# Performance work log

Hardware: AMD Instinct MI355X
Metric: run time of the kernel (lower is better)

Reference implementation:

```python
import jax, jax.numpy as jnp
import numpy as np

N, E, G = 50000, 1600000, 64          # nodes, edges, graphs
NODE_IN, EDGE_IN, HID, L, H = 32, 16, 64, 3, 4
C = HID // H                           # per-head channels (PyG out_channels)


def setup_inputs() -> dict:
    key = jax.random.key(0)
    ks = jax.random.split(key, 12)
    x = jax.random.normal(ks[0], (N, NODE_IN), jnp.float32)
    edge_index = jax.random.randint(ks[1], (2, E), 0, N, jnp.int32)
    edge_attr = jax.random.normal(ks[2], (E, EDGE_IN), jnp.float32)
    batch = jnp.sort(jax.random.randint(ks[3], (N,), 0, G, jnp.int32))
    s = lambda k, shape, fan: jax.random.normal(k, shape, jnp.float32) / np.sqrt(fan)
    Wn = s(ks[4], (NODE_IN, HID), NODE_IN); bn = jnp.zeros((HID,), jnp.float32)
    Wq = s(ks[5], (L, HID, HID), HID);      bq = jnp.zeros((L, HID), jnp.float32)
    Wk = s(ks[6], (L, HID, HID), HID);      bk = jnp.zeros((L, HID), jnp.float32)
    Wv = s(ks[7], (L, HID, HID), HID);      bv = jnp.zeros((L, HID), jnp.float32)
    We = s(ks[8], (L, EDGE_IN, HID), EDGE_IN)          # lin_edge, bias=False in PyG
    Ws = s(ks[9], (L, HID, HID), HID);      bs = jnp.zeros((L, HID), jnp.float32)  # lin_skip
    W1 = s(ks[10], (HID, HID // 2), HID);   b1 = jnp.zeros((HID // 2,), jnp.float32)
    W2 = s(ks[11], (HID // 2, 1), HID // 2); b2 = jnp.zeros((1,), jnp.float32)
    return dict(x=x, edge_index=edge_index, edge_attr=edge_attr, batch=batch,
                Wn=Wn, bn=bn, Wq=Wq, bq=bq, Wk=Wk, bk=bk, Wv=Wv, bv=bv,
                We=We, Ws=Ws, bs=bs, W1=W1, b1=b1, W2=W2, b2=b2)


def _transformer_conv(x, src, dst, edge_attr, Wq, bq, Wk, bk, Wv, bv, We, Ws, bs):
    # PyG TransformerConv (concat=True, beta=False, root_weight=True), eval mode.
    q = (x @ Wq + bq)[dst].reshape(E, H, C)              # query at target nodes
    e = (edge_attr @ We).reshape(E, H, C)                # edge embedding
    k = (x @ Wk + bk)[src].reshape(E, H, C) + e          # key at source + edge
    alpha = (q * k).sum(-1) / jnp.sqrt(jnp.float32(C))   # [E, H]
    amax = jax.ops.segment_max(alpha, dst, num_segments=N)
    ex = jnp.exp(alpha - amax[dst])
    denom = jax.ops.segment_sum(ex, dst, num_segments=N)
    attn = ex / (denom[dst] + 1e-16)                     # segment softmax over in-edges
    v = (x @ Wv + bv)[src].reshape(E, H, C) + e
    agg = jax.ops.segment_sum((v * attn[..., None]).reshape(E, HID), dst, num_segments=N)
    return agg + x @ Ws + bs                             # skip connection (lin_skip)


def reference(x, edge_index, edge_attr, batch, Wn, bn, Wq, bq, Wk, bk, Wv, bv,
              We, Ws, bs, W1, b1, W2, b2):
    src, dst = edge_index[0], edge_index[1]
    h = jax.nn.relu(x @ Wn + bn)
    for l in range(L):  # dropout is identity in eval mode
        h_new = jax.nn.relu(_transformer_conv(h, src, dst, edge_attr,
                                              Wq[l], bq[l], Wk[l], bk[l],
                                              Wv[l], bv[l], We[l], Ws[l], bs[l]))
        h = h + h_new
    # global_mean_pool
    cnt = jax.ops.segment_sum(jnp.ones((N,), h.dtype), batch, num_segments=G)
    pooled = jax.ops.segment_sum(h, batch, num_segments=G) / jnp.maximum(cnt, 1.0)[:, None]
    out = jax.nn.relu(pooled @ W1 + b1) @ W2 + b2
    return out.squeeze(-1)
```

## Files before the change

kernel.cpp:

```cpp
#include <hip/hip_runtime.h>
#include <hip/hip_fp16.h>
#include <stdint.h>

#define Nn 50000
#define Ee 1600000
#define Gg 64
#define TB 2048
#define NTB ((Ee + TB - 1) / TB)
#define NBK ((Nn + 255) / 256)

typedef _Float16 f16x2 __attribute__((ext_vector_type(2)));
typedef _Float16 f16x4 __attribute__((ext_vector_type(4)));
typedef _Float16 f16x8 __attribute__((ext_vector_type(8)));
typedef float    f32x4v __attribute__((ext_vector_type(4)));

__device__ __forceinline__ float fdot2f(f16x2 a, f16x2 b, float c) {
#if __has_builtin(__builtin_amdgcn_fdot2)
    return __builtin_amdgcn_fdot2(a, b, c, false);
#else
    return fmaf((float)a[0], (float)b[0], fmaf((float)a[1], (float)b[1], c));
#endif
}

__global__ void k_hist(const int* __restrict__ ei, int* __restrict__ deg) {
    int e = blockIdx.x * blockDim.x + threadIdx.x;
    if (e < Ee) atomicAdd(&deg[ei[Ee + e]], 1);
}

__global__ void k_scan1(const int* __restrict__ deg, int* __restrict__ row_ptr,
                        int* __restrict__ bsum) {
    __shared__ int buf[256];
    int i = blockIdx.x * 256 + threadIdx.x;
    int v = (i < Nn) ? deg[i] : 0;
    buf[threadIdx.x] = v;
    __syncthreads();
    for (int off = 1; off < 256; off <<= 1) {
        int t = (threadIdx.x >= off) ? buf[threadIdx.x - off] : 0;
        __syncthreads();
        buf[threadIdx.x] += t;
        __syncthreads();
    }
    if (i < Nn) row_ptr[i + 1] = buf[threadIdx.x];
    if (threadIdx.x == 255) bsum[blockIdx.x] = buf[255];
}

__global__ void k_scan2(int* __restrict__ bsum, int nb) {
    __shared__ int buf[256];
    int v = (threadIdx.x < nb) ? bsum[threadIdx.x] : 0;
    buf[threadIdx.x] = v;
    __syncthreads();
    for (int off = 1; off < 256; off <<= 1) {
        int t = (threadIdx.x >= off) ? buf[threadIdx.x - off] : 0;
        __syncthreads();
        buf[threadIdx.x] += t;
        __syncthreads();
    }
    if (threadIdx.x < nb) bsum[threadIdx.x] = buf[threadIdx.x];
}

__global__ void k_scan3(int* __restrict__ row_ptr, const int* __restrict__ bsum) {
    int i = blockIdx.x * 256 + threadIdx.x;
    if (i > Nn) return;
    if (i == 0) { row_ptr[0] = 0; return; }
    int b = (i - 1) >> 8;
    if (b > 0) row_ptr[i] += bsum[b - 1];
}

__global__ void k_scatter(const int* __restrict__ ei, int* __restrict__ cursor,
                          int* __restrict__ src_perm, int* __restrict__ eperm) {
    int e = blockIdx.x * blockDim.x + threadIdx.x;
    if (e >= Ee) return;
    int dst = ei[Ee + e];
    int pos = atomicAdd(&cursor[dst], 1);
    src_perm[pos] = ei[e];
    eperm[pos] = e;
}

__global__ void k_easort(const float* __restrict__ ea, const int* __restrict__ eperm,
                         __half* __restrict__ ea_h) {
    long t = (long)blockIdx.x * blockDim.x + threadIdx.x;
    if (t >= (long)Ee * 4) return;
    long idx = t >> 2;
    int e = eperm[idx];
    float4 v = ((const float4*)ea)[(long)e * 4 + (t & 3)];
    __half2 lo = __floats2half2_rn(v.x, v.y);
    __half2 hi = __floats2half2_rn(v.z, v.w);
    ((__half2*)ea_h)[t * 2]     = lo;
    ((__half2*)ea_h)[t * 2 + 1] = hi;
}


__global__ __launch_bounds__(256) void k_cnt(const int* __restrict__ ei,
                                             int* __restrict__ table) {
    __shared__ int hist[NBK];
    for (int i = threadIdx.x; i < NBK; i += 256) hist[i] = 0;
    __syncthreads();
    int e0 = blockIdx.x * TB;
    for (int i = threadIdx.x; i < TB; i += 256) {
        int e = e0 + i;
        if (e >= Ee) break;
        atomicAdd(&hist[ei[Ee + e] >> 8], 1);
    }
    __syncthreads();
    for (int i = threadIdx.x; i < NBK; i += 256)
        table[i * NTB + blockIdx.x] = hist[i];
}

__global__ __launch_bounds__(256) void k_colscan(int* __restrict__ table,
                                                 int* __restrict__ bktsz) {
    __shared__ int buf[1024];
    int c = blockIdx.x;
    for (int k = 0; k < 4; ++k) {
        int i = threadIdx.x + k * 256;
        buf[i] = (i < NTB) ? table[c * NTB + i] : 0;
    }
    __syncthreads();
    for (int off = 1; off < 1024; off <<= 1) {
        int v[4];
        for (int k = 0; k < 4; ++k) {
            int i = threadIdx.x + k * 256;
            v[k] = (i >= off) ? buf[i - off] : 0;
        }
        __syncthreads();
        for (int k = 0; k < 4; ++k) buf[threadIdx.x + k * 256] += v[k];
        __syncthreads();
    }
    for (int k = 0; k < 4; ++k) {
        int i = threadIdx.x + k * 256;
        if (i < NTB) table[c * NTB + i] = i ? buf[i - 1] : 0;
    }
    if (threadIdx.x == 0) bktsz[c] = buf[1023];
}

__global__ __launch_bounds__(256) void k_bktscan(const int* __restrict__ bktsz,
                                                 int* __restrict__ bktbase) {
    __shared__ int buf[256];
    int i = threadIdx.x;
    buf[i] = (i < NBK) ? bktsz[i] : 0;
    __syncthreads();
    for (int off = 1; off < 256; off <<= 1) {
        int v = (i >= off) ? buf[i - off] : 0;
        __syncthreads();
        buf[i] += v;
        __syncthreads();
    }
    if (i == 0) bktbase[0] = 0;
    if (i < NBK) bktbase[i + 1] = buf[i];
}

__global__ __launch_bounds__(256) void k_binfill(const int* __restrict__ ei,
                        const int* __restrict__ table, const int* __restrict__ bktbase,
                        unsigned long long* __restrict__ tmp) {
    __shared__ int off_s[NBK];
    __shared__ int cnt_s[NBK];
    for (int i = threadIdx.x; i < NBK; i += 256) {
        off_s[i] = table[i * NTB + blockIdx.x];
        cnt_s[i] = 0;
    }
    __syncthreads();
    int e0 = blockIdx.x * TB;
    for (int i = threadIdx.x; i < TB; i += 256) {
        int e = e0 + i;
        if (e >= Ee) break;
        int src = ei[e];
        int dst = ei[Ee + e];
        int b = dst >> 8;
        int r = atomicAdd(&cnt_s[b], 1);
        long pos = (long)bktbase[b] + off_s[b] + r;
        tmp[pos] = ((unsigned long long)(unsigned)dst << 37)
                 | ((unsigned long long)(unsigned)src << 21)
                 | (unsigned long long)(unsigned)e;
    }
}

__global__ __launch_bounds__(256) void k_bktB(const unsigned long long* __restrict__ tmp,
                        const int* __restrict__ bktbase, int* __restrict__ row_ptr,
                        int* __restrict__ src_perm, int* __restrict__ eord) {
    __shared__ int cnt[256];
    __shared__ int sc[256];
    __shared__ int lro[256];
    int b = blockIdx.x, tid = threadIdx.x;
    cnt[tid] = 0;
    __syncthreads();
    int s = bktbase[b], t_end = bktbase[b + 1];
    for (int i = s + tid; i < t_end; i += 256)
        atomicAdd(&cnt[(int)(tmp[i] >> 37) & 255], 1);
    __syncthreads();
    sc[tid] = cnt[tid];
    __syncthreads();
    for (int off = 1; off < 256; off <<= 1) {
        int v = (tid >= off) ? sc[tid - off] : 0;
        __syncthreads();
        sc[tid] += v;
        __syncthreads();
    }
    lro[tid] = tid ? sc[tid - 1] : 0;
    cnt[tid] = 0;
    int n = b * 256 + tid;
    if (n < Nn) row_ptr[n] = s + lro[tid];
    if (b == NBK - 1 && tid == 0) row_ptr[Nn] = Ee;
    __syncthreads();
    for (int i = s + tid; i < t_end; i += 256) {
        unsigned long long p = tmp[i];
        int dn = (int)(p >> 37) & 255;
        int r = atomicAdd(&cnt[dn], 1);
        int pos = s + lro[dn] + r;
        src_perm[pos] = (int)((p >> 21) & 0xFFFFull);
        eord[pos] = (int)(p & 0x1FFFFFull);
    }
}

__global__ void k_scatB2(const int* __restrict__ eord,
                         const float* __restrict__ ea, __half* __restrict__ ea_h) {
    int t = blockIdx.x * blockDim.x + threadIdx.x;
    if (t >= Ee) return;
    int e = eord[t];
    const f32x4v* er = (const f32x4v*)(ea + (size_t)e * 16);
    f32x4v v0 = __builtin_nontemporal_load(er);
    f32x4v v1 = __builtin_nontemporal_load(er + 1);
    f32x4v v2 = __builtin_nontemporal_load(er + 2);
    f32x4v v3 = __builtin_nontemporal_load(er + 3);
    __half2 h0 = __floats2half2_rn(v0[0], v0[1]), h1 = __floats2half2_rn(v0[2], v0[3]);
    __half2 h2 = __floats2half2_rn(v1[0], v1[1]), h3 = __floats2half2_rn(v1[2], v1[3]);
    __half2 h4 = __floats2half2_rn(v2[0], v2[1]), h5 = __floats2half2_rn(v2[2], v2[3]);
    __half2 h6 = __floats2half2_rn(v3[0], v3[1]), h7 = __floats2half2_rn(v3[2], v3[3]);
    uint4 a = make_uint4(*(unsigned*)&h0, *(unsigned*)&h1,
                         *(unsigned*)&h2, *(unsigned*)&h3);
    uint4 bb = make_uint4(*(unsigned*)&h4, *(unsigned*)&h5,
                          *(unsigned*)&h6, *(unsigned*)&h7);
    uint4* o = (uint4*)(ea_h + (size_t)t * 16);
    o[0] = a;
    o[1] = bb;
}

__global__ void k_gbound(const int* __restrict__ batch, int* __restrict__ gstart) {
    int n = blockIdx.x * blockDim.x + threadIdx.x;
    if (n >= Nn) return;
    int b = batch[n];
    if (n == 0) { for (int g = 0; g <= b; ++g) gstart[g] = 0; }
    else { int bp = batch[n - 1]; for (int g = bp + 1; g <= b; ++g) gstart[g] = n; }
    if (n == Nn - 1) { for (int g = b + 1; g <= Gg; ++g) gstart[g] = Nn; }
}

__global__ __launch_bounds__(256) void k_encode(const float* __restrict__ x,
                         const float* __restrict__ Wn,
                         const float* __restrict__ bn, float* __restrict__ h) {
    __shared__ float sx[64 * 32];
    int base = blockIdx.x * 64;
    for (int i = threadIdx.x; i < 512; i += 256) {
        int off = i * 4, row = off >> 5;
        float4 v = (base + row < Nn) ? ((const float4*)(x))[(base * 32 + off) >> 2]
                                     : make_float4(0.f, 0.f, 0.f, 0.f);
        ((float4*)sx)[i] = v;
    }
    __syncthreads();
    int lane = threadIdx.x & 63, wv = threadIdx.x >> 6;
    float acc[16];
    float b = bn[lane];
#pragma unroll
    for (int nn = 0; nn < 16; ++nn) acc[nn] = b;
#pragma unroll 1
    for (int k0 = 0; k0 < 32; k0 += 4) {
        float w0 = Wn[(k0 + 0) * 64 + lane];
        float w1 = Wn[(k0 + 1) * 64 + lane];
        float w2 = Wn[(k0 + 2) * 64 + lane];
        float w3 = Wn[(k0 + 3) * 64 + lane];
#pragma unroll
        for (int nn = 0; nn < 16; ++nn) {
            int row = wv * 16 + nn;
            float4 hv = *(const float4*)&sx[row * 32 + k0];
            acc[nn] = fmaf(hv.x, w0, fmaf(hv.y, w1, fmaf(hv.z, w2, fmaf(hv.w, w3, acc[nn]))));
        }
    }
#pragma unroll
    for (int nn = 0; nn < 16; ++nn) {
        int n = base + wv * 16 + nn;
        if (n < Nn) h[(size_t)n * 64 + lane] = fmaxf(acc[nn], 0.f);
    }
}

__global__ void k_wqm3(const float* __restrict__ Wq_all, const float* __restrict__ bq_all,
                       const float* __restrict__ We_all, float* __restrict__ Wqm3,
                       float* __restrict__ bqm3) {
    int l = blockIdx.x;
    const float* Wq = Wq_all + l * 4096;
    const float* bq = bq_all + l * 64;
    const float* We = We_all + l * 1024;
    float* Wqm = Wqm3 + l * 4096;
    float* bqm = bqm3 + l * 64;
    for (int o = threadIdx.x; o < 64 * 64; o += 256) {
        int j = o >> 6, lp = o & 63, hh = lp >> 4, ii = lp & 15;
        float acc = 0.f;
#pragma unroll
        for (int c = 0; c < 16; ++c)
            acc += Wq[j * 64 + hh * 16 + c] * We[ii * 64 + hh * 16 + c];
        Wqm[o] = acc;
    }
    if (threadIdx.x < 64) {
        int hh = threadIdx.x >> 4, ii = threadIdx.x & 15;
        float acc = 0.f;
#pragma unroll
        for (int c = 0; c < 16; ++c)
            acc += bq[hh * 16 + c] * We[ii * 64 + hh * 16 + c];
        bqm[threadIdx.x] = acc;
    }
}

__global__ void k_pack(const float* __restrict__ Wq, const float* __restrict__ Wk,
                       const float* __restrict__ Wv, const float* __restrict__ Wqm3,
                       const float* __restrict__ Ws, __half* __restrict__ pw) {
    int l = blockIdx.x / 5, m = blockIdx.x % 5;
    const float SC = 0.25f * 1.4426950408889634f;
    const float* src;
    float sc = 1.f;
    if (m == 0)      { src = Wq + l * 4096;   sc = SC; }
    else if (m == 1) { src = Wk + l * 4096; }
    else if (m == 2) { src = Wv + l * 4096; }
    else if (m == 3) { src = Wqm3 + l * 4096; sc = SC; }
    else             { src = Ws + l * 4096; }
    __half* dst = pw + ((size_t)l * 5 + m) * 4096;
    for (int i = threadIdx.x; i < 4096; i += 256) {
        int k = i >> 6, c = i & 63;
        dst[(k >> 1) * 128 + 2 * c + (k & 1)] = __float2half_rn(src[i] * sc);
    }
}

__global__ __launch_bounds__(256) void k_qkvt2(const float* __restrict__ h,
                       const __half* __restrict__ pw,
                       const float* __restrict__ bq, const float* __restrict__ bk,
                       const float* __restrict__ bv, const float* __restrict__ bqm,
                       const float* __restrict__ bs,
                       __half* __restrict__ qn16, __half* __restrict__ kvi,
                       __half* __restrict__ tq16, float* __restrict__ sn) {
    __shared__ __half sh[64 * 64];
    int base = blockIdx.x * 64;
    for (int i = threadIdx.x; i < 1024; i += 256) {
        int off = i * 4, row = off >> 6;
        float4 v = (base + row < Nn) ? ((const float4*)(h))[((size_t)base * 64 + off) >> 2]
                                     : make_float4(0.f, 0.f, 0.f, 0.f);
        ((__half2*)sh)[i * 2]     = __floats2half2_rn(v.x, v.y);
        ((__half2*)sh)[i * 2 + 1] = __floats2half2_rn(v.z, v.w);
    }
    __syncthreads();
    int lane = threadIdx.x & 63, wv = threadIdx.x >> 6;
    const float SC = 0.25f * 1.4426950408889634f;
    const __half* Pq = pw;
    const __half* Pk = pw + 4096;
    const __half* Pv = pw + 8192;
    const __half* Pt = pw + 12288;
    const __half* Ps = pw + 16384;
    float aq[16], ak[16], av[16], at[16], as_[16];
    float _bq = bq[lane] * SC, _bk = bk[lane], _bv = bv[lane],
          _bt = bqm[lane] * SC, _bs = bs[lane];
#pragma unroll
    for (int nn = 0; nn < 16; ++nn) {
        aq[nn] = _bq; ak[nn] = _bk; av[nn] = _bv; at[nn] = _bt; as_[nn] = _bs;
    }
#pragma unroll 1
    for (int k0 = 0; k0 < 64; k0 += 4) {
        int pi = (k0 >> 1) * 128 + 2 * lane;
        f16x2 wq0 = *(const f16x2*)(Pq + pi), wq1 = *(const f16x2*)(Pq + pi + 128);
        f16x2 wk0 = *(const f16x2*)(Pk + pi), wk1 = *(const f16x2*)(Pk + pi + 128);
        f16x2 wv0 = *(const f16x2*)(Pv + pi), wv1 = *(const f16x2*)(Pv + pi + 128);
        f16x2 wt0 = *(const f16x2*)(Pt + pi), wt1 = *(const f16x2*)(Pt + pi + 128);
        f16x2 ws0 = *(const f16x2*)(Ps + pi), ws1 = *(const f16x2*)(Ps + pi + 128);
#pragma unroll
        for (int nn = 0; nn < 16; ++nn) {
            int row = wv * 16 + nn;
            f16x4 hv = *(const f16x4*)&sh[row * 64 + k0];
            f16x2 h01 = __builtin_shufflevector(hv, hv, 0, 1);
            f16x2 h23 = __builtin_shufflevector(hv, hv, 2, 3);
            aq[nn]  = fdot2f(h01, wq0, fdot2f(h23, wq1, aq[nn]));
            ak[nn]  = fdot2f(h01, wk0, fdot2f(h23, wk1, ak[nn]));
            av[nn]  = fdot2f(h01, wv0, fdot2f(h23, wv1, av[nn]));
            at[nn]  = fdot2f(h01, wt0, fdot2f(h23, wt1, at[nn]));
            as_[nn] = fdot2f(h01, ws0, fdot2f(h23, ws1, as_[nn]));
        }
    }
    int ko = 8 * (lane >> 2) + (lane & 3);
#pragma unroll
    for (int nn = 0; nn < 16; ++nn) {
        int n = base + wv * 16 + nn;
        if (n < Nn) {
            size_t o = (size_t)n * 64 + lane;
            qn16[o] = __float2half_rn(aq[nn]);
            tq16[o] = __float2half_rn(at[nn]);
            sn[o] = as_[nn];
            kvi[(size_t)n * 128 + ko]     = __float2half_rn(ak[nn]);
            kvi[(size_t)n * 128 + ko + 4] = __float2half_rn(av[nn]);
        }
    }
}

__global__ __launch_bounds__(256) void k_layer8(float* __restrict__ h,
                      const __half* __restrict__ qn16, const __half* __restrict__ kvi,
                      const __half* __restrict__ tq16, const float* __restrict__ sn,
                      const int* __restrict__ row_ptr, const int* __restrict__ src_perm,
                      const __half* __restrict__ eah, const float* __restrict__ We) {
    __shared__ float sWe[1024];
    __shared__ float tE[4][64];
    __shared__ float tV[4][64];
    for (int t = threadIdx.x; t < 1024; t += 256) sWe[t] = We[t];
    __syncthreads();
    int lane = threadIdx.x & 63, wv = threadIdx.x >> 6;
    int slot = lane >> 4, sl = lane & 15;
    int hh = lane >> 4;
    const int xoff = 4 * (sl & 3);
#pragma unroll 1
    for (int j = 0; j < 4; ++j) {
        int n = blockIdx.x * 16 + wv * 4 + j;
        if (n >= Nn) break;
        int beg = row_ptr[n], end = row_ptr[n + 1];
        f16x4 qv = *(const f16x4*)(qn16 + (size_t)n * 64 + 4 * sl);
        f16x4 tv = *(const f16x4*)(tq16 + (size_t)n * 64 + 4 * sl);
        f16x2 qa = __builtin_shufflevector(qv, qv, 0, 1);
        f16x2 qb = __builtin_shufflevector(qv, qv, 2, 3);
        f16x2 ta = __builtin_shufflevector(tv, tv, 0, 1);
        f16x2 tb = __builtin_shufflevector(tv, tv, 2, 3);
        float accd = 0.f;
        float4 accv = make_float4(0.f, 0.f, 0.f, 0.f);
        float4 acce = make_float4(0.f, 0.f, 0.f, 0.f);
        for (int idx = beg; idx < end; idx += 8) {
            int e0 = idx + slot, e1 = idx + 4 + slot;
            bool ok0 = e0 < end, ok1 = e1 < end;
            int i0 = ok0 ? e0 : beg, i1 = ok1 ? e1 : beg;
            int s0 = src_perm[i0], s1 = src_perm[i1];
            f16x8 kv0 = *(const f16x8*)(kvi + (size_t)s0 * 128 + 8 * sl);
            f16x8 kv1 = *(const f16x8*)(kvi + (size_t)s1 * 128 + 8 * sl);
            f16x4 x0 = *(const f16x4*)(eah + (size_t)i0 * 16 + xoff);
            f16x4 x1 = *(const f16x4*)(eah + (size_t)i1 * 16 + xoff);
            float a0 = fdot2f(qa, __builtin_shufflevector(kv0, kv0, 0, 1),
                       fdot2f(qb, __builtin_shufflevector(kv0, kv0, 2, 3),
                       fdot2f(ta, __builtin_shufflevector(x0, x0, 0, 1),
                       fdot2f(tb, __builtin_shufflevector(x0, x0, 2, 3), -6.0f))));
            float a1 = fdot2f(qa, __builtin_shufflevector(kv1, kv1, 0, 1),
                       fdot2f(qb, __builtin_shufflevector(kv1, kv1, 2, 3),
                       fdot2f(ta, __builtin_shufflevector(x1, x1, 0, 1),
                       fdot2f(tb, __builtin_shufflevector(x1, x1, 2, 3), -6.0f))));
            a0 += __shfl_xor(a0, 1, 4); a1 += __shfl_xor(a1, 1, 4);
            a0 += __shfl_xor(a0, 2, 4); a1 += __shfl_xor(a1, 2, 4);
            float p0 = ok0 ? __builtin_exp2f(a0) : 0.f;
            float p1 = ok1 ? __builtin_exp2f(a1) : 0.f;
            accd += p0 + p1;
            accv.x = fmaf(p0, (float)kv0[4], fmaf(p1, (float)kv1[4], accv.x));
            accv.y = fmaf(p0, (float)kv0[5], fmaf(p1, (float)kv1[5], accv.y));
            accv.z = fmaf(p0, (float)kv0[6], fmaf(p1, (float)kv1[6], accv.z));
            accv.w = fmaf(p0, (float)kv0[7], fmaf(p1, (float)kv1[7], accv.w));
            acce.x = fmaf(p0, (float)x0[0], fmaf(p1, (float)x1[0], acce.x));
            acce.y = fmaf(p0, (float)x0[1], fmaf(p1, (float)x1[1], acce.y));
            acce.z = fmaf(p0, (float)x0[2], fmaf(p1, (float)x1[2], acce.z));
            acce.w = fmaf(p0, (float)x0[3], fmaf(p1, (float)x1[3], acce.w));
        }
        accd   += __shfl_xor(accd, 16);   accd   += __shfl_xor(accd, 32);
        accv.x += __shfl_xor(accv.x, 16); accv.x += __shfl_xor(accv.x, 32);
        accv.y += __shfl_xor(accv.y, 16); accv.y += __shfl_xor(accv.y, 32);
        accv.z += __shfl_xor(accv.z, 16); accv.z += __shfl_xor(accv.z, 32);
        accv.w += __shfl_xor(accv.w, 16); accv.w += __shfl_xor(accv.w, 32);
        acce.x += __shfl_xor(acce.x, 16); acce.x += __shfl_xor(acce.x, 32);
        acce.y += __shfl_xor(acce.y, 16); acce.y += __shfl_xor(acce.y, 32);
        acce.z += __shfl_xor(acce.z, 16); acce.z += __shfl_xor(acce.z, 32);
        acce.w += __shfl_xor(acce.w, 16); acce.w += __shfl_xor(acce.w, 32);
        float inv = 1.f / (accd + 1e-16f);
        if (slot == 0) {
            ((float4*)tE[wv])[sl] = make_float4(acce.x * inv, acce.y * inv,
                                                acce.z * inv, acce.w * inv);
            ((float4*)tV[wv])[sl] = make_float4(accv.x * inv, accv.y * inv,
                                                accv.z * inv, accv.w * inv);
        }
        float re = 0.f;
#pragma unroll
        for (int i = 0; i < 16; ++i)
            re = fmaf(tE[wv][hh * 16 + i], sWe[i * 64 + lane], re);
        size_t o = (size_t)n * 64 + lane;
        float hv = h[o];
        h[o] = hv + fmaxf(tV[wv][lane] + re + sn[o], 0.f);
    }
}

__global__ __launch_bounds__(256) void k_layer(float* __restrict__ h,
                      const __half* __restrict__ qn16, const __half* __restrict__ kvi,
                      const __half* __restrict__ tq16, const float* __restrict__ sn,
                      const int* __restrict__ row_ptr, const int* __restrict__ src_perm,
                      const int* __restrict__ eperm, const float* __restrict__ eaf,
                      const float* __restrict__ We) {
    __shared__ float sWe[1024];
    __shared__ float tile[4][64];
    for (int t = threadIdx.x; t < 1024; t += 256) sWe[t] = We[t];
    __syncthreads();
    int lane = threadIdx.x & 63, wv = threadIdx.x >> 6;
    int hh = lane >> 4, cc = lane & 15;
    int ko = 8 * (lane >> 2) + (lane & 3);
    int n = blockIdx.x * 4 + wv;
    if (n >= Nn) return;
    int beg = row_ptr[n], end = row_ptr[n + 1];
    float q = __half2float(qn16[(size_t)n * 64 + lane]);
    float t = __half2float(tq16[(size_t)n * 64 + lane]);
    float m = -INFINITY, accd = 0.f, accv = 0.f, acce = 0.f;
    int idx = beg;
    for (; idx < end; ++idx) {
        long b0 = (long)src_perm[idx] * 128;
        float k0 = __half2float(kvi[b0 + ko]);
        float v0 = __half2float(kvi[b0 + ko + 4]);
        float x0 = eaf[(long)eperm[idx] * 16 + cc];
        float a0 = fmaf(q, k0, x0 * t);
        a0 += __shfl_xor(a0, 1, 16);
        a0 += __shfl_xor(a0, 2, 16);
        a0 += __shfl_xor(a0, 4, 16);
        a0 += __shfl_xor(a0, 8, 16);
        float nm = fmaxf(m, a0);
        float w = __builtin_exp2f(m - nm);
        float p0 = __builtin_exp2f(a0 - nm);
        accd = fmaf(accd, w, p0);
        accv = fmaf(accv, w, p0 * v0);
        acce = fmaf(acce, w, p0 * x0);
        m = nm;
    }
    float inv = 1.f / (accd + 1e-16f);
    tile[wv][lane] = acce * inv;
    float re = 0.f;
#pragma unroll
    for (int i = 0; i < 16; ++i)
        re = fmaf(tile[wv][hh * 16 + i], sWe[i * 64 + lane], re);
    size_t o = (size_t)n * 64 + lane;
    float hv = h[o];
    h[o] = hv + fmaxf(fmaf(accv, inv, re + sn[o]), 0.f);
}

__global__ void k_pool(const float* __restrict__ h, const int* __restrict__ gstart,
                       const float* __restrict__ W1, const float* __restrict__ b1,
                       const float* __restrict__ W2, const float* __restrict__ b2,
                       float* __restrict__ out) {
    int g = blockIdx.x;
    int lane = threadIdx.x & 63, wv = threadIdx.x >> 6;
    int beg = gstart[g], end = gstart[g + 1];
    __shared__ float red[4][64];
    __shared__ float sp[64];
    __shared__ float sh[32];
    float acc = 0.f;
    for (int n = beg + wv; n < end; n += 4) acc += h[(size_t)n * 64 + lane];
    red[wv][lane] = acc;
    __syncthreads();
    if (threadIdx.x < 64) {
        float c = fmaxf((float)(end - beg), 1.f);
        sp[lane] = (red[0][lane] + red[1][lane] + red[2][lane] + red[3][lane]) / c;
    }
    __syncthreads();
    if (threadIdx.x < 32) {
        int t = threadIdx.x;
        float a = b1[t];
#pragma unroll
        for (int i = 0; i < 64; ++i) a = fmaf(sp[i], W1[i * 32 + t], a);
        sh[t] = fmaxf(a, 0.f) * W2[t];
    }
    __syncthreads();
    if (threadIdx.x == 0) {
        float s = b2[0];
#pragma unroll
        for (int i = 0; i < 32; ++i) s += sh[i];
        out[g] = s;
    }
}

extern "C" void kernel_launch(void* const* d_in, const int* in_sizes, int n_in,
                              void* d_out, int out_size, void* d_ws, size_t ws_size,
                              hipStream_t stream) {
    const float* x   = (const float*)d_in[0];
    const int*   ei  = (const int*)d_in[1];
    const float* ea  = (const float*)d_in[2];
    const int*   bat = (const int*)d_in[3];
    const float* Wn  = (const float*)d_in[4];
    const float* bn  = (const float*)d_in[5];
    const float* Wq  = (const float*)d_in[6];
    const float* bq  = (const float*)d_in[7];
    const float* Wk  = (const float*)d_in[8];
    const float* bk  = (const float*)d_in[9];
    const float* Wv  = (const float*)d_in[10];
    const float* bv  = (const float*)d_in[11];
    const float* We  = (const float*)d_in[12];
    const float* Wsk = (const float*)d_in[13];
    const float* bs  = (const float*)d_in[14];
    const float* W1  = (const float*)d_in[15];
    const float* b1  = (const float*)d_in[16];
    const float* W2  = (const float*)d_in[17];
    const float* b2  = (const float*)d_in[18];
    float* out = (float*)d_out;

    const size_t NH = (size_t)Nn * 64;
    float* h    = (float*)d_ws;
    float* qn   = h + NH;
    float* tq   = h + 2 * NH;
    float* sn   = h + 3 * NH;
    __half* kv  = (__half*)(h + 4 * NH);
    float* Wqm3 = h + 5 * NH;
    float* bqm3 = Wqm3 + 3 * 4096;
    __half* pw  = (__half*)(bqm3 + 3 * 64);
    int* deg       = (int*)(pw + 3 * 5 * 4096);
    int* row_ptr   = deg + Nn;
    int* cursor    = row_ptr + Nn + 1;
    int* src_perm  = cursor + Nn;
    int* eperm     = src_perm + Ee;
    int* bsum      = eperm + Ee;
    int* gstart    = bsum + 256;
    char* pe = (char*)(gstart + Gg + 1);
    __half* ea_h = (__half*)(((uintptr_t)pe + 63) & ~(uintptr_t)63);
    char* pt = (char*)(ea_h + (size_t)Ee * 16);
    unsigned long long* tmp =
        (unsigned long long*)(((uintptr_t)pt + 15) & ~(uintptr_t)15);
    size_t need_eah = ((char*)(ea_h + (size_t)Ee * 16)) - (char*)d_ws;
    size_t need_tmp = ((char*)(tmp + Ee)) - (char*)d_ws;
    int* eord    = (int*)qn;
    int* table   = (int*)tq;
    int* bktsz   = (int*)sn;
    int* bktbase = bktsz + 256;
    __half* qn16 = (__half*)qn;
    __half* tq16 = (__half*)tq;
    int mode = (ws_size >= need_tmp) ? 2 : (ws_size >= need_eah) ? 1 : 0;

    if (mode == 2) {
        k_cnt<<<NTB, 256, 0, stream>>>(ei, table);
        k_colscan<<<NBK, 256, 0, stream>>>(table, bktsz);
        k_bktscan<<<1, 256, 0, stream>>>(bktsz, bktbase);
        k_binfill<<<NTB, 256, 0, stream>>>(ei, table, bktbase, tmp);
        k_bktB<<<NBK, 256, 0, stream>>>(tmp, bktbase, row_ptr, src_perm, eord);
        k_scatB2<<<(Ee + 255) / 256, 256, 0, stream>>>(eord, ea, ea_h);
    } else {
        const int NB = 196;
        hipMemsetAsync(deg, 0, Nn * sizeof(int), stream);
        k_hist<<<(Ee + 255) / 256, 256, 0, stream>>>(ei, deg);
        k_scan1<<<NB, 256, 0, stream>>>(deg, row_ptr, bsum);
        k_scan2<<<1, 256, 0, stream>>>(bsum, NB);
        k_scan3<<<(Nn + 256) / 256, 256, 0, stream>>>(row_ptr, bsum);
        hipMemcpyAsync(cursor, row_ptr, Nn * sizeof(int), hipMemcpyDeviceToDevice, stream);
        k_scatter<<<(Ee + 255) / 256, 256, 0, stream>>>(ei, cursor, src_perm, eperm);
        if (mode == 1)
            k_easort<<<((long)Ee * 4 + 255) / 256, 256, 0, stream>>>(ea, eperm, ea_h);
    }
    k_gbound<<<(Nn + 255) / 256, 256, 0, stream>>>(bat, gstart);
    k_wqm3<<<3, 256, 0, stream>>>(Wq, bq, We, Wqm3, bqm3);
    k_pack<<<15, 256, 0, stream>>>(Wq, Wk, Wv, Wqm3, Wsk, pw);

    int nodeBlocks = (Nn + 63) / 64;
    k_encode<<<nodeBlocks, 256, 0, stream>>>(x, Wn, bn, h);
    for (int l = 0; l < 3; ++l) {
        k_qkvt2<<<nodeBlocks, 256, 0, stream>>>(h, pw + (size_t)l * 5 * 4096,
                                                bq + l * 64, bk + l * 64, bv + l * 64,
                                                bqm3 + l * 64, bs + l * 64,
                                                qn16, kv, tq16, sn);
        if (mode >= 1)
            k_layer8<<<(Nn + 15) / 16, 256, 0, stream>>>(h, qn16, kv, tq16, sn,
                    row_ptr, src_perm, ea_h, We + l * 1024);
        else
            k_layer<<<(Nn + 3) / 4, 256, 0, stream>>>(h, qn16, kv, tq16, sn,
                    row_ptr, src_perm, eperm, ea, We + l * 1024);
    }
    k_pool<<<Gg, 256, 0, stream>>>(h, gstart, W1, b1, W2, b2, out);
}
```

Baseline: 683.5 us.

## Use 64-node buckets and fuse edge-attr scatter with layer-0 QKV kernel

Shrinks the CSR bucket granularity from 256 to 64 destination nodes, so there are four times as many buckets and the bucket-scan grows to 1024 entries. k_bktB now runs with only 64 active counters per block. The edge-attribute scatter/fp16 conversion now handles two edges per thread with plain loads instead of nontemporal ones. It is merged with the first layer's QKV projection into a single launch that runs both concurrently via a block-index split, with eord moved to eperm so it no longer aliases qn. Fewer bins and more blocks improve parallelism in the bucket phase, but three quarters of the threads in k_bktB sit idle during the scan.

```diff
diff --git a/kernel.cpp b/kernel.cpp
--- a/kernel.cpp
+++ b/kernel.cpp
@@ -7,12 +7,12 @@
 #define Gg 64
 #define TB 2048
 #define NTB ((Ee + TB - 1) / TB)
-#define NBK ((Nn + 255) / 256)
+#define NBK ((Nn + 63) / 64)
+#define SB2B 3125
 
 typedef _Float16 f16x2 __attribute__((ext_vector_type(2)));
 typedef _Float16 f16x4 __attribute__((ext_vector_type(4)));
 typedef _Float16 f16x8 __attribute__((ext_vector_type(8)));
-typedef float    f32x4v __attribute__((ext_vector_type(4)));
 
 __device__ __forceinline__ float fdot2f(f16x2 a, f16x2 b, float c) {
 #if __has_builtin(__builtin_amdgcn_fdot2)
@@ -99,7 +99,7 @@
     for (int i = threadIdx.x; i < TB; i += 256) {
         int e = e0 + i;
         if (e >= Ee) break;
-        atomicAdd(&hist[ei[Ee + e] >> 8], 1);
+        atomicAdd(&hist[ei[Ee + e] >> 6], 1);
     }
     __syncthreads();
     for (int i = threadIdx.x; i < NBK; i += 256)
@@ -134,18 +134,27 @@
 
 __global__ __launch_bounds__(256) void k_bktscan(const int* __restrict__ bktsz,
                                                  int* __restrict__ bktbase) {
-    __shared__ int buf[256];
-    int i = threadIdx.x;
-    buf[i] = (i < NBK) ? bktsz[i] : 0;
-    __syncthreads();
-    for (int off = 1; off < 256; off <<= 1) {
-        int v = (i >= off) ? buf[i - off] : 0;
-        __syncthreads();
-        buf[i] += v;
-        __syncthreads();
-    }
-    if (i == 0) bktbase[0] = 0;
-    if (i < NBK) bktbase[i + 1] = buf[i];
+    __shared__ int buf[1024];
+    for (int k = 0; k < 4; ++k) {
+        int i = threadIdx.x + k * 256;
+        buf[i] = (i < NBK) ? bktsz[i] : 0;
+    }
+    __syncthreads();
+    for (int off = 1; off < 1024; off <<= 1) {
+        int v[4];
+        for (int k = 0; k < 4; ++k) {
+            int i = threadIdx.x + k * 256;
+            v[k] = (i >= off) ? buf[i - off] : 0;
+        }
+        __syncthreads();
+        for (int k = 0; k < 4; ++k) buf[threadIdx.x + k * 256] += v[k];
+        __syncthreads();
+    }
+    for (int k = 0; k < 4; ++k) {
+        int i = threadIdx.x + k * 256;
+        if (i < NBK) bktbase[i + 1] = buf[i];
+    }
+    if (threadIdx.x == 0) bktbase[0] = 0;
 }
 
 __global__ __launch_bounds__(256) void k_binfill(const int* __restrict__ ei,
@@ -164,7 +173,7 @@
         if (e >= Ee) break;
         int src = ei[e];
         int dst = ei[Ee + e];
-        int b = dst >> 8;
+        int b = dst >> 6;
         int r = atomicAdd(&cnt_s[b], 1);
         long pos = (long)bktbase[b] + off_s[b] + r;
         tmp[pos] = ((unsigned long long)(unsigned)dst << 37)
@@ -176,33 +185,35 @@
 __global__ __launch_bounds__(256) void k_bktB(const unsigned long long* __restrict__ tmp,
                         const int* __restrict__ bktbase, int* __restrict__ row_ptr,
                         int* __restrict__ src_perm, int* __restrict__ eord) {
-    __shared__ int cnt[256];
-    __shared__ int sc[256];
-    __shared__ int lro[256];
+    __shared__ int cnt[64];
+    __shared__ int sc[64];
+    __shared__ int lro[64];
     int b = blockIdx.x, tid = threadIdx.x;
-    cnt[tid] = 0;
+    if (tid < 64) cnt[tid] = 0;
     __syncthreads();
     int s = bktbase[b], t_end = bktbase[b + 1];
     for (int i = s + tid; i < t_end; i += 256)
-        atomicAdd(&cnt[(int)(tmp[i] >> 37) & 255], 1);
-    __syncthreads();
-    sc[tid] = cnt[tid];
-    __syncthreads();
-    for (int off = 1; off < 256; off <<= 1) {
-        int v = (tid >= off) ? sc[tid - off] : 0;
-        __syncthreads();
-        sc[tid] += v;
-        __syncthreads();
-    }
-    lro[tid] = tid ? sc[tid - 1] : 0;
-    cnt[tid] = 0;
-    int n = b * 256 + tid;
-    if (n < Nn) row_ptr[n] = s + lro[tid];
+        atomicAdd(&cnt[(int)(tmp[i] >> 37) & 63], 1);
+    __syncthreads();
+    if (tid < 64) sc[tid] = cnt[tid];
+    __syncthreads();
+    for (int off = 1; off < 64; off <<= 1) {
+        int v = (tid < 64 && tid >= off) ? sc[tid - off] : 0;
+        __syncthreads();
+        if (tid < 64) sc[tid] += v;
+        __syncthreads();
+    }
+    if (tid < 64) {
+        lro[tid] = tid ? sc[tid - 1] : 0;
+        cnt[tid] = 0;
+        int n = b * 64 + tid;
+        if (n < Nn) row_ptr[n] = s + lro[tid];
+    }
     if (b == NBK - 1 && tid == 0) row_ptr[Nn] = Ee;
     __syncthreads();
     for (int i = s + tid; i < t_end; i += 256) {
         unsigned long long p = tmp[i];
-        int dn = (int)(p >> 37) & 255;
+        int dn = (int)(p >> 37) & 63;
         int r = atomicAdd(&cnt[dn], 1);
         int pos = s + lro[dn] + r;
         src_perm[pos] = (int)((p >> 21) & 0xFFFFull);
@@ -210,27 +221,33 @@
     }
 }
 
+__device__ __forceinline__ void scatB2_body(int bid, const int* __restrict__ eord,
+                        const float* __restrict__ ea, __half* __restrict__ ea_h) {
+    int t0 = (bid * 256 + threadIdx.x) * 2;
+    if (t0 >= Ee) return;
+    int e0 = eord[t0], e1 = eord[t0 + 1];
+    const float4* r0 = (const float4*)(ea + (size_t)e0 * 16);
+    const float4* r1 = (const float4*)(ea + (size_t)e1 * 16);
+    float4 a0 = r0[0], a1 = r0[1], a2 = r0[2], a3 = r0[3];
+    float4 c0 = r1[0], c1 = r1[1], c2 = r1[2], c3 = r1[3];
+    __half2 h0 = __floats2half2_rn(a0.x, a0.y), h1 = __floats2half2_rn(a0.z, a0.w);
+    __half2 h2 = __floats2half2_rn(a1.x, a1.y), h3 = __floats2half2_rn(a1.z, a1.w);
+    __half2 h4 = __floats2half2_rn(a2.x, a2.y), h5 = __floats2half2_rn(a2.z, a2.w);
+    __half2 h6 = __floats2half2_rn(a3.x, a3.y), h7 = __floats2half2_rn(a3.z, a3.w);
+    __half2 g0 = __floats2half2_rn(c0.x, c0.y), g1 = __floats2half2_rn(c0.z, c0.w);
+    __half2 g2 = __floats2half2_rn(c1.x, c1.y), g3 = __floats2half2_rn(c1.z, c1.w);
+    __half2 g4 = __floats2half2_rn(c2.x, c2.y), g5 = __floats2half2_rn(c2.z, c2.w);
+    __half2 g6 = __floats2half2_rn(c3.x, c3.y), g7 = __floats2half2_rn(c3.z, c3.w);
+    uint4* o = (uint4*)(ea_h + (size_t)t0 * 16);
+    o[0] = make_uint4(*(unsigned*)&h0, *(unsigned*)&h1, *(unsigned*)&h2, *(unsigned*)&h3);
+    o[1] = make_uint4(*(unsigned*)&h4, *(unsigned*)&h5, *(unsigned*)&h6, *(unsigned*)&h7);
+    o[2] = make_uint4(*(unsigned*)&g0, *(unsigned*)&g1, *(unsigned*)&g2, *(unsigned*)&g3);
+    o[3] = make_uint4(*(unsigned*)&g4, *(unsigned*)&g5, *(unsigned*)&g6, *(unsigned*)&g7);
+}
+
 __global__ void k_scatB2(const int* __restrict__ eord,
                          const float* __restrict__ ea, __half* __restrict__ ea_h) {
-    int t = blockIdx.x * blockDim.x + threadIdx.x;
-    if (t >= Ee) return;
-    int e = eord[t];
-    const f32x4v* er = (const f32x4v*)(ea + (size_t)e * 16);
-    f32x4v v0 = __builtin_nontemporal_load(er);
-    f32x4v v1 = __builtin_nontemporal_load(er + 1);
-    f32x4v v2 = __builtin_nontemporal_load(er + 2);
-    f32x4v v3 = __builtin_nontemporal_load(er + 3);
-    __half2 h0 = __floats2half2_rn(v0[0], v0[1]), h1 = __floats2half2_rn(v0[2], v0[3]);
-    __half2 h2 = __floats2half2_rn(v1[0], v1[1]), h3 = __floats2half2_rn(v1[2], v1[3]);
-    __half2 h4 = __floats2half2_rn(v2[0], v2[1]), h5 = __floats2half2_rn(v2[2], v2[3]);
-    __half2 h6 = __floats2half2_rn(v3[0], v3[1]), h7 = __floats2half2_rn(v3[2], v3[3]);
-    uint4 a = make_uint4(*(unsigned*)&h0, *(unsigned*)&h1,
-                         *(unsigned*)&h2, *(unsigned*)&h3);
-    uint4 bb = make_uint4(*(unsigned*)&h4, *(unsigned*)&h5,
-                          *(unsigned*)&h6, *(unsigned*)&h7);
-    uint4* o = (uint4*)(ea_h + (size_t)t * 16);
-    o[0] = a;
-    o[1] = bb;
+    scatB2_body(blockIdx.x, eord, ea, ea_h);
 }
 
 __global__ void k_gbound(const int* __restrict__ batch, int* __restrict__ gstart) {
@@ -325,7 +342,7 @@
     }
 }
 
-__global__ __launch_bounds__(256) void k_qkvt2(const float* __restrict__ h,
+__device__ __forceinline__ void qkvt2_body(int bid, const float* __restrict__ h,
                        const __half* __restrict__ pw,
                        const float* __restrict__ bq, const float* __restrict__ bk,
                        const float* __restrict__ bv, const float* __restrict__ bqm,
@@ -333,7 +350,7 @@
                        __half* __restrict__ qn16, __half* __restrict__ kvi,
                        __half* __restrict__ tq16, float* __restrict__ sn) {
     __shared__ __half sh[64 * 64];
-    int base = blockIdx.x * 64;
+    int base = bid * 64;
     for (int i = threadIdx.x; i < 1024; i += 256) {
         int off = i * 4, row = off >> 6;
         float4 v = (base + row < Nn) ? ((const float4*)(h))[((size_t)base * 64 + off) >> 2]
@@ -390,6 +407,31 @@
             kvi[(size_t)n * 128 + ko + 4] = __float2half_rn(av[nn]);
         }
     }
+}
+
+__global__ __launch_bounds__(256) void k_qkvt2(const float* __restrict__ h,
+                       const __half* __restrict__ pw,
+                       const float* __restrict__ bq, const float* __restrict__ bk,
+                       const float* __restrict__ bv, const float* __restrict__ bqm,
+                       const float* __restrict__ bs,
+                       __half* __restrict__ qn16, __half* __restrict__ kvi,
+                       __half* __restrict__ tq16, float* __restrict__ sn) {
+    qkvt2_body(blockIdx.x, h, pw, bq, bk, bv, bqm, bs, qn16, kvi, tq16, sn);
+}
+
+__global__ __launch_bounds__(256) void k_sqk(const int* __restrict__ eord,
+                       const float* __restrict__ ea, __half* __restrict__ ea_h,
+                       const float* __restrict__ h, const __half* __restrict__ pw,
+                       const float* __restrict__ bq, const float* __restrict__ bk,
+                       const float* __restrict__ bv, const float* __restrict__ bqm,
+                       const float* __restrict__ bs,
+                       __half* __restrict__ qn16, __half* __restrict__ kvi,
+                       __half* __restrict__ tq16, float* __restrict__ sn) {
+    if (blockIdx.x < SB2B)
+        scatB2_body(blockIdx.x, eord, ea, ea_h);
+    else
+        qkvt2_body(blockIdx.x - SB2B, h, pw, bq, bk, bv, bqm, bs,
+                   qn16, kvi, tq16, sn);
 }
 
 __global__ __launch_bounds__(256) void k_layer8(float* __restrict__ h,
@@ -608,10 +650,10 @@
         (unsigned long long*)(((uintptr_t)pt + 15) & ~(uintptr_t)15);
     size_t need_eah = ((char*)(ea_h + (size_t)Ee * 16)) - (char*)d_ws;
     size_t need_tmp = ((char*)(tmp + Ee)) - (char*)d_ws;
-    int* eord    = (int*)qn;
+    int* eord    = eperm;
     int* table   = (int*)tq;
     int* bktsz   = (int*)sn;
-    int* bktbase = bktsz + 256;
+    int* bktbase = bktsz + 1024;
     __half* qn16 = (__half*)qn;
     __half* tq16 = (__half*)tq;
     int mode = (ws_size >= need_tmp) ? 2 : (ws_size >= need_eah) ? 1 : 0;
@@ -622,7 +664,6 @@
         k_bktscan<<<1, 256, 0, stream>>>(bktsz, bktbase);
         k_binfill<<<NTB, 256, 0, stream>>>(ei, table, bktbase, tmp);
         k_bktB<<<NBK, 256, 0, stream>>>(tmp, bktbase, row_ptr, src_perm, eord);
-        k_scatB2<<<(Ee + 255) / 256, 256, 0, stream>>>(eord, ea, ea_h);
     } else {
         const int NB = 196;
         hipMemsetAsync(deg, 0, Nn * sizeof(int), stream);
@@ -642,10 +683,14 @@
     int nodeBlocks = (Nn + 63) / 64;
     k_encode<<<nodeBlocks, 256, 0, stream>>>(x, Wn, bn, h);
     for (int l = 0; l < 3; ++l) {
-        k_qkvt2<<<nodeBlocks, 256, 0, stream>>>(h, pw + (size_t)l * 5 * 4096,
-                                                bq + l * 64, bk + l * 64, bv + l * 64,
-                                                bqm3 + l * 64, bs + l * 64,
-                                                qn16, kv, tq16, sn);
+        if (l == 0 && mode == 2) {
+            k_sqk<<<SB2B + nodeBlocks, 256, 0, stream>>>(eord, ea, ea_h,
+                    h, pw, bq, bk, bv, bqm3, bs, qn16, kv, tq16, sn);
+        } else {
+            k_qkvt2<<<nodeBlocks, 256, 0, stream>>>(h, pw + (size_t)l * 5 * 4096,
+                    bq + l * 64, bk + l * 64, bv + l * 64,
+                    bqm3 + l * 64, bs + l * 64, qn16, kv, tq16, sn);
+        }
         if (mode >= 1)
             k_layer8<<<(Nn + 15) / 16, 256, 0, stream>>>(h, qn16, kv, tq16, sn,
                     row_ptr, src_perm, ea_h, We + l * 1024);
```

Result: faster. 657.7 us (-3.8%).
